# Optimization experiments

Measured on AMD Instinct MI355X. Metric: run time of the kernel, lower is better.

## Reference

```python
import jax, jax.numpy as jnp
import numpy as np

B = 16384
N_NODES = 55
N = B * N_NODES
IN_CH = 13
HID = 32
MAX_NBR = 6
N_LAYERS = 5
E = 4 * N


def _sage(x, src, dst, wl, bl, wr, n):
    # PyG SAGEConv: out = lin_l(mean_j x_j) + lin_r(x_i); lin_l has bias, lin_r does not.
    msgs = x[src]                                                   # [E, d]
    agg = jax.ops.segment_sum(msgs, dst, num_segments=n)            # [N, d]
    cnt = jax.ops.segment_sum(jnp.ones((src.shape[0],), x.dtype), dst, num_segments=n)
    agg = agg / jnp.maximum(cnt, 1.0)[:, None]
    return agg @ wl + bl + x @ wr


def setup_inputs() -> dict:
    key = jax.random.key(0)
    ks = jax.random.split(key, 24)
    x = jax.random.normal(ks[0], (N, IN_CH), dtype=jnp.float32)
    # column -3 (index 10) is a binary neighbor mask: exactly MAX_NBR ones per graph
    u = jax.random.uniform(ks[1], (B, N_NODES))
    nbr_idx = jnp.argsort(u, axis=1)[:, :MAX_NBR]
    mask = jnp.zeros((B, N_NODES), jnp.float32).at[jnp.arange(B)[:, None], nbr_idx].set(1.0)
    x = x.at[:, IN_CH - 3].set(mask.reshape(-1))
    edge_index = jax.random.randint(ks[2], (2, E), 0, N, dtype=jnp.int64)
    shuffle_indices = jax.random.randint(ks[3], (B, MAX_NBR), 0, MAX_NBR, dtype=jnp.int64)
    s = 0.1
    wl0 = jax.random.normal(ks[4], (IN_CH, HID)) * s
    bl0 = jnp.zeros((HID,), jnp.float32)
    wr0 = jax.random.normal(ks[5], (IN_CH, HID)) * s
    wl = jax.random.normal(ks[6], (N_LAYERS - 1, HID, HID)) * s
    bl = jnp.zeros((N_LAYERS - 1, HID), jnp.float32)
    wr = jax.random.normal(ks[7], (N_LAYERS - 1, HID, HID)) * s
    wq = jax.random.normal(ks[8], (HID, HID)) * s
    bq = jnp.zeros((HID,), jnp.float32)
    wk = jax.random.normal(ks[9], (HID, HID)) * s
    bk = jnp.zeros((HID,), jnp.float32)
    wv = jax.random.normal(ks[10], (HID, HID)) * s
    bv = jnp.zeros((HID,), jnp.float32)
    wo = jax.random.normal(ks[11], (HID, HID)) * s
    bo = jnp.zeros((HID,), jnp.float32)
    w_fc = jax.random.normal(ks[12], (HID * MAX_NBR, MAX_NBR)) * s
    b_fc = jnp.zeros((MAX_NBR,), jnp.float32)
    return {"x": x, "edge_index": edge_index, "shuffle_indices": shuffle_indices,
            "wl0": wl0, "bl0": bl0, "wr0": wr0, "wl": wl, "bl": bl, "wr": wr,
            "wq": wq, "bq": bq, "wk": wk, "bk": bk, "wv": wv, "bv": bv,
            "wo": wo, "bo": bo, "w_fc": w_fc, "b_fc": b_fc}


def reference(x, edge_index, shuffle_indices, wl0, bl0, wr0, wl, bl, wr,
              wq, bq, wk, bk, wv, bv, wo, bo, w_fc, b_fc):
    n = x.shape[0]
    b = n // N_NODES
    src, dst = edge_index[0], edge_index[1]
    nbr_mask = x[:, IN_CH - 3].reshape(b, N_NODES)                  # [B, 55]

    h = jax.nn.selu(_sage(x, src, dst, wl0, bl0, wr0, n))
    jk = h
    for i in range(N_LAYERS - 1):
        h = jax.nn.selu(_sage(h, src, dst, wl[i], bl[i], wr[i], n))
        jk = jnp.maximum(jk, h)                                     # JumpingKnowledge('max')

    h = jax.nn.selu(jk)                                             # [N, HID]
    keys = h.reshape(b, N_NODES, HID)
    values = keys

    # dynamic neighbor gather: indices of mask==1 in ascending order, zero-padded to MAX_NBR
    order = jnp.argsort(-nbr_mask, axis=1, stable=True)[:, :MAX_NBR]  # [B, 6]
    barange = jnp.arange(b)[:, None]
    query = keys[barange, order]                                    # [B, 6, HID]
    valid = jnp.take_along_axis(nbr_mask, order, axis=1) > 0.5      # [B, 6] bool
    query = jnp.where(valid[..., None], query, 0.0)
    query = query[barange, shuffle_indices]                         # shuffled gather

    # single-head cross attention (head_dim = HID)
    Q = query @ wq + bq
    K = keys @ wk + bk
    V = values @ wv + bv
    scores = jnp.einsum('bqd,bkd->bqk', Q, K) / jnp.sqrt(jnp.float32(HID))
    attn = jax.nn.softmax(scores, axis=-1)
    out = jnp.einsum('bqk,bkd->bqd', attn, V) @ wo + bo             # [B, 6, HID]

    out = jax.nn.selu(out.reshape(b, HID * MAX_NBR))
    return out @ w_fc + b_fc                                        # [B, 6]
```

## Files before the change

### kernel.cpp

```cpp
#include <hip/hip_runtime.h>
#include <cstdint>
#include <cstddef>

#define NODES   55
#define BGRAPH  16384
#define NTOT    (BGRAPH*NODES)
#define INCH    13
#define HID     32
#define ETOT    (4*NTOT)
#define NPB     128
#define ECAP    768
#define ZN      NTOT

#define NBUCK   220
#define BSH     12
#define BMSK    4095
#define NBLK    2048
#define BCAP2   32
#define BINTH   256
#define BINGRP  (ETOT/4/NBLK)
#define OVFCAP  8192

#define ASTR    72
#define BSTR    72
#define ASTR0   40

typedef _Float16 f16;
typedef _Float16 f16x4 __attribute__((ext_vector_type(4)));
typedef _Float16 f16x8 __attribute__((ext_vector_type(8)));
typedef float    f32x4 __attribute__((ext_vector_type(4)));

__device__ __forceinline__ float selu_f(float v){
  const float s  = 1.0507009873554805f;
  const float sa = 1.7580993408473766f;
  return v > 0.f ? s*v : sa*(__expf(v)-1.f);
}

__global__ __launch_bounds__(256) void k_pad(const float* __restrict__ x,
                                             float* __restrict__ xf,
                                             uint32_t* __restrict__ ha32,
                                             int* __restrict__ ocnt){
  if (blockIdx.x == 0){
    int t = threadIdx.x;
    if (t == 0) *ocnt = 0;
    if (t < 16)            xf[(size_t)ZN*16 + t] = 0.f;
    if (t >= 16 && t < 32) ha32[(size_t)ZN*16 + (t-16)] = 0u;
  }
  int i = blockIdx.x*256 + threadIdx.x;
  int node = i>>2, q = i&3;
  const float* r = x + (size_t)node*INCH + q*4;
  float4 v;
  v.x = r[0];
  v.y = (q<3) ? r[1] : 0.f;
  v.z = (q<3) ? r[2] : 0.f;
  v.w = (q<3) ? r[3] : 0.f;
  ((float4*)xf)[i] = v;
}

__global__ __launch_bounds__(256) void k_wprep(
    const float* __restrict__ wl0, const float* __restrict__ wr0,
    const float* __restrict__ wl,  const float* __restrict__ wr,
    f16* __restrict__ wcp)
{
  int t = threadIdx.x;
  for (int i=t; i<1024; i+=256){
    int oc = i>>5, k = i&31;
    float v = 0.f;
    if (k < 13)                 v = wl0[k*HID + oc];
    else if (k >= 16 && k < 29) v = wr0[(k-16)*HID + oc];
    wcp[oc*32 + k] = (f16)v;
  }
  for (int i=t; i<4*2048; i+=256){
    int l = i>>11, r = i&2047, oc = r>>6, k = r&63;
    float v = (k<32) ? wl[l*1024 + k*HID + oc] : wr[l*1024 + (k-32)*HID + oc];
    wcp[1024 + l*2048 + oc*64 + k] = (f16)v;
  }
}

__global__ __launch_bounds__(BINTH) void k_bin(
    const int* __restrict__ src, const int* __restrict__ dst,
    uint32_t* __restrict__ binned, int* __restrict__ gcnt,
    uint2* __restrict__ ovf, int* __restrict__ ocnt)
{
  __shared__ int lcnt[NBUCK];
  int t = threadIdx.x, bid = blockIdx.x;
  for (int i=t;i<NBUCK;i+=BINTH) lcnt[i]=0;
  __syncthreads();
  const int4* s4 = (const int4*)src;
  const int4* d4 = (const int4*)dst;
  int g0 = bid*BINGRP;
  for (int i=t; i<BINGRP; i+=BINTH){
    int4 s = s4[g0+i];
    int4 d = d4[g0+i];
    #pragma unroll
    for (int j=0;j<4;j++){
      int dd = (&d.x)[j];
      int ss = (&s.x)[j];
      int b  = dd >> BSH;
      uint32_t entry = (uint32_t)ss | ((uint32_t)(dd & BMSK) << 20);
      int pos = atomicAdd(&lcnt[b], 1);
      if (pos < BCAP2) binned[((size_t)b*NBLK + bid)*BCAP2 + pos] = entry;
      else {
        int gp = atomicAdd(ocnt, 1);
        if (gp < OVFCAP) ovf[gp] = make_uint2(entry, (uint32_t)b);
      }
    }
  }
  __syncthreads();
  for (int i=t;i<NBUCK;i+=BINTH){
    int c = lcnt[i]; if (c > BCAP2) c = BCAP2;
    gcnt[bid*NBUCK + i] = c;
  }
}

__global__ __launch_bounds__(256) void k_btot(const int* __restrict__ gcnt,
                                              const uint2* __restrict__ ovf,
                                              const int* __restrict__ ocnt,
                                              int* __restrict__ btot){
  __shared__ int sd[256];
  int b = blockIdx.x, t = threadIdx.x;
  int s = 0;
  for (int i=t;i<NBLK;i+=256) s += gcnt[i*NBUCK + b];
  int oc = *ocnt; if (oc > OVFCAP) oc = OVFCAP;
  for (int j=t;j<oc;j+=256) if (ovf[j].y == (uint32_t)b) s++;
  sd[t]=s; __syncthreads();
  for (int o=128;o>0;o>>=1){ if (t<o) sd[t]+=sd[t+o]; __syncthreads(); }
  if (t==0) btot[b]=sd[0];
}

__global__ __launch_bounds__(256) void k_bscan(const int* __restrict__ btot,
                                               int* __restrict__ bbase){
  __shared__ int sd[256];
  int t = threadIdx.x;
  int v = (t<NBUCK) ? btot[t] : 0;
  sd[t] = v; __syncthreads();
  for (int o=1;o<256;o<<=1){
    int u = (t>=o) ? sd[t-o] : 0;
    __syncthreads();
    sd[t] += u;
    __syncthreads();
  }
  if (t<NBUCK) bbase[t] = sd[t] - v;
}

__global__ __launch_bounds__(1024) void k_bucket(
    const uint32_t* __restrict__ binned, const int* __restrict__ gcnt,
    const int* __restrict__ bbase,
    const uint2* __restrict__ ovf, const int* __restrict__ ocnt,
    int* __restrict__ off, uint32_t* __restrict__ csrp)
{
  __shared__ int hist[4096];
  __shared__ int cnts[NBLK];
  __shared__ int ws[1024];
  int b = blockIdx.x, t = threadIdx.x;
  int base = bbase[b];
  for (int i=t;i<NBLK;i+=1024) cnts[i] = gcnt[i*NBUCK + b];
  #pragma unroll
  for (int i=0;i<4;i++) hist[t+1024*i] = 0;
  int oc = *ocnt; if (oc > OVFCAP) oc = OVFCAP;
  __syncthreads();

  const uint4* bb4 = (const uint4*)(binned + (size_t)b*(NBLK*BCAP2));
  for (int i=t; i<NBLK*BCAP2/4; i+=1024){
    uint4 e = bb4[i];
    int c = cnts[i>>3];
    int s0 = (i&7)*4;
    if (s0   < c) atomicAdd(&hist[(e.x>>20)&BMSK],1);
    if (s0+1 < c) atomicAdd(&hist[(e.y>>20)&BMSK],1);
    if (s0+2 < c) atomicAdd(&hist[(e.z>>20)&BMSK],1);
    if (s0+3 < c) atomicAdd(&hist[(e.w>>20)&BMSK],1);
  }
  for (int j=t;j<oc;j+=1024){
    uint2 pr = ovf[j];
    if (pr.y == (uint32_t)b) atomicAdd(&hist[(pr.x>>20)&BMSK],1);
  }
  __syncthreads();
  int t4 = t*4;
  int s0=hist[t4], s1=hist[t4+1], s2=hist[t4+2], s3=hist[t4+3];
  int sum = s0+s1+s2+s3;
  ws[t] = sum; __syncthreads();
  for (int o=1;o<1024;o<<=1){
    int u = (t>=o) ? ws[t-o] : 0;
    __syncthreads();
    ws[t] += u;
    __syncthreads();
  }
  int ex = ws[t] - sum;
  int p0 = ex, p1 = ex+s0, p2 = ex+s0+s1, p3 = ex+s0+s1+s2;
  hist[t4]=p0; hist[t4+1]=p1; hist[t4+2]=p2; hist[t4+3]=p3;
  int4 ov; ov.x = base+p0; ov.y = base+p1; ov.z = base+p2; ov.w = base+p3;
  ((int4*)(off + (b<<BSH)))[t] = ov;
  if (b == NBUCK-1 && t == 1023) off[NTOT] = ETOT;
  __syncthreads();
  for (int i=t; i<NBLK*BCAP2/4; i+=1024){
    uint4 e = bb4[i];
    int c = cnts[i>>3];
    int s0b = (i&7)*4;
    int p;
    if (s0b   < c){ p = atomicAdd(&hist[(e.x>>20)&BMSK],1); csrp[base+p] = e.x & 0xFFFFFu; }
    if (s0b+1 < c){ p = atomicAdd(&hist[(e.y>>20)&BMSK],1); csrp[base+p] = e.y & 0xFFFFFu; }
    if (s0b+2 < c){ p = atomicAdd(&hist[(e.z>>20)&BMSK],1); csrp[base+p] = e.z & 0xFFFFFu; }
    if (s0b+3 < c){ p = atomicAdd(&hist[(e.w>>20)&BMSK],1); csrp[base+p] = e.w & 0xFFFFFu; }
  }
  for (int j=t;j<oc;j+=1024){
    uint2 pr = ovf[j];
    if (pr.y == (uint32_t)b){
      int p = atomicAdd(&hist[(pr.x>>20)&BMSK],1);
      csrp[base+p] = pr.x & 0xFFFFFu;
    }
  }
}

__global__ __launch_bounds__(256,8) void k_layer0(
    const float* __restrict__ xf,
    const int* __restrict__ off, const uint32_t* __restrict__ csrp,
    const f16* __restrict__ wcat0, const float* __restrict__ bl0,
    f16* __restrict__ hout, f16* __restrict__ jkout)
{
  __shared__ uint32_t ALDS[NPB*(ASTR0/2)];
  __shared__ uint32_t BLDS[32*(ASTR0/2)];
  __shared__ uint32_t EL[ECAP];
  __shared__ int      sOFF[NPB+2];
  __shared__ float    biasL[32];
  int t = threadIdx.x;
  int base = blockIdx.x*NPB;
  int e0 = off[base];
  int e1 = off[base+NPB];
  for (int i=t; i<NPB+1; i+=256) sOFF[i] = off[base+i];
  {
    int lim = (e1-e0) < ECAP ? (e1-e0) : ECAP;
    for (int i=t; i<lim; i+=256) EL[i] = csrp[e0+i];
  }
  if (t < 128){
    int oc = t>>2, kq = (t&3)*8;
    f16x8 wv = *(const f16x8*)(wcat0 + oc*32 + kq);
    *(f16x8*)((f16*)BLDS + oc*ASTR0 + kq) = wv;
  }
  if (t < 32) biasL[t] = bl0[t];
  __syncthreads();

  int c4 = t & 3;
  #pragma unroll
  for (int p=0;p<2;p++){
    int nl = p*64 + (t>>2);
    int node = base + nl;
    float4 xown = *((const float4*)(xf + (size_t)node*16) + c4);
    int s = sOFF[nl] - e0;
    int d = sOFF[nl+1] - sOFF[nl];
    float a0=0.f,a1=0.f,a2=0.f,a3=0.f;
    for (int i=0;i<d;i+=4){
      int j0 = s+i;
      uint32_t k0,k1,k2,k3;
      if (j0+3 < ECAP){ k0=EL[j0]; k1=EL[j0+1]; k2=EL[j0+2]; k3=EL[j0+3]; }
      else            { k0=csrp[e0+j0]; k1=csrp[e0+j0+1]; k2=csrp[e0+j0+2]; k3=csrp[e0+j0+3]; }
      k1 = (i+1<d)?k1:(uint32_t)ZN;
      k2 = (i+2<d)?k2:(uint32_t)ZN;
      k3 = (i+3<d)?k3:(uint32_t)ZN;
      float4 g0 = *((const float4*)(xf + (size_t)k0*16u) + c4);
      float4 g1 = *((const float4*)(xf + (size_t)k1*16u) + c4);
      float4 g2 = *((const float4*)(xf + (size_t)k2*16u) + c4);
      float4 g3 = *((const float4*)(xf + (size_t)k3*16u) + c4);
      a0 += (g0.x+g1.x)+(g2.x+g3.x);
      a1 += (g0.y+g1.y)+(g2.y+g3.y);
      a2 += (g0.z+g1.z)+(g2.z+g3.z);
      a3 += (g0.w+g1.w)+(g2.w+g3.w);
    }
    float inv = 1.f/(float)(d<1?1:d);
    union { f16 h[4]; uint32_t u[2]; } mp, xp;
    mp.h[0]=(f16)(a0*inv); mp.h[1]=(f16)(a1*inv); mp.h[2]=(f16)(a2*inv); mp.h[3]=(f16)(a3*inv);
    xp.h[0]=(f16)xown.x;   xp.h[1]=(f16)xown.y;   xp.h[2]=(f16)xown.z;   xp.h[3]=(f16)xown.w;
    uint32_t* arow = &ALDS[nl*(ASTR0/2)];
    *((uint2*)&arow[2*c4])     = make_uint2(mp.u[0], mp.u[1]);
    *((uint2*)&arow[8 + 2*c4]) = make_uint2(xp.u[0], xp.u[1]);
  }
  __syncthreads();

  int w = t>>6, l = t&63;
  int lrow = l&15, lg = l>>4;
  const f16* Af = (const f16*)ALDS;
  const f16* Bf = (const f16*)BLDS;
  f32x4 D00={0.f,0.f,0.f,0.f}, D01=D00, D10=D00, D11=D00;
  {
    f16x8 af0 = *(const f16x8*)(Af + (32*w+lrow)*ASTR0    + 8*lg);
    f16x8 af1 = *(const f16x8*)(Af + (32*w+16+lrow)*ASTR0 + 8*lg);
    f16x8 bf0 = *(const f16x8*)(Bf + lrow*ASTR0           + 8*lg);
    f16x8 bf1 = *(const f16x8*)(Bf + (16+lrow)*ASTR0      + 8*lg);
    D00 = __builtin_amdgcn_mfma_f32_16x16x32_f16(af0, bf0, D00, 0,0,0);
    D01 = __builtin_amdgcn_mfma_f32_16x16x32_f16(af0, bf1, D01, 0,0,0);
    D10 = __builtin_amdgcn_mfma_f32_16x16x32_f16(af1, bf0, D10, 0,0,0);
    D11 = __builtin_amdgcn_mfma_f32_16x16x32_f16(af1, bf1, D11, 0,0,0);
  }
  __syncthreads();

  f16* ST = (f16*)ALDS;
  #pragma unroll
  for (int j=0;j<4;j++){
    int r0 = 32*w + 4*lg + j, r1 = r0 + 16;
    ST[r0*34 + lrow]      = (f16)selu_f(D00[j] + biasL[lrow]);
    ST[r0*34 + 16 + lrow] = (f16)selu_f(D01[j] + biasL[16+lrow]);
    ST[r1*34 + lrow]      = (f16)selu_f(D10[j] + biasL[lrow]);
    ST[r1*34 + 16 + lrow] = (f16)selu_f(D11[j] + biasL[16+lrow]);
  }
  __syncthreads();

  const uint32_t* STd = (const uint32_t*)ALDS;
  uint4* ho4 = (uint4*)hout;
  uint4* jo4 = (uint4*)jkout;
  int gbase = blockIdx.x*(NPB*HID/8);
  #pragma unroll
  for (int k=0;k<2;k++){
    int cch = t + 256*k;
    int n = cch>>2, m = cch&3;
    int dd = n*17 + m*4;
    uint4 u;
    u.x=STd[dd]; u.y=STd[dd+1]; u.z=STd[dd+2]; u.w=STd[dd+3];
    ho4[gbase+cch] = u;
    jo4[gbase+cch] = u;
  }
}

__global__ __launch_bounds__(256,6) void k_layer(
    const f16* __restrict__ hin,
    const int* __restrict__ off, const uint32_t* __restrict__ csrp,
    const f16* __restrict__ wcat, const float* __restrict__ bl,
    f16* __restrict__ hout, f16* __restrict__ jkio)
{
  __shared__ uint32_t ALDS[NPB*(ASTR/2)];
  __shared__ uint32_t BLDS[32*(BSTR/2)];
  __shared__ uint32_t EL[ECAP];
  __shared__ int      sOFF[NPB+2];
  __shared__ float    biasL[32];
  int t = threadIdx.x;
  int base = blockIdx.x*NPB;
  int e0 = off[base];
  int e1 = off[base+NPB];
  for (int i=t; i<NPB+1; i+=256) sOFF[i] = off[base+i];
  {
    int lim = (e1-e0) < ECAP ? (e1-e0) : ECAP;
    for (int i=t; i<lim; i+=256) EL[i] = csrp[e0+i];
  }
  if (t < 128){
    int oc = t>>2, kq = (t&3)*8;
    f16x8 wv0 = *(const f16x8*)(wcat + oc*64 + kq);
    f16x8 wv1 = *(const f16x8*)(wcat + oc*64 + 32 + kq);
    *(f16x8*)((f16*)BLDS + oc*BSTR + kq)      = wv0;
    *(f16x8*)((f16*)BLDS + oc*BSTR + 32 + kq) = wv1;
  }
  if (t < 32) biasL[t] = bl[t];
  __syncthreads();

  int c4 = t & 3;
  #pragma unroll
  for (int p=0;p<2;p++){
    int nl = p*64 + (t>>2);
    int node = base + nl;
    f16x8 hown = *(const f16x8*)(hin + (size_t)node*HID + 8u*c4);
    int s = sOFF[nl] - e0;
    int d = sOFF[nl+1] - sOFF[nl];
    float a[8];
    #pragma unroll
    for (int r=0;r<8;r++) a[r]=0.f;
    for (int i=0;i<d;i+=4){
      int j0 = s+i;
      uint32_t k0,k1,k2,k3;
      if (j0+3 < ECAP){ k0=EL[j0]; k1=EL[j0+1]; k2=EL[j0+2]; k3=EL[j0+3]; }
      else            { k0=csrp[e0+j0]; k1=csrp[e0+j0+1]; k2=csrp[e0+j0+2]; k3=csrp[e0+j0+3]; }
      k1 = (i+1<d)?k1:(uint32_t)ZN;
      k2 = (i+2<d)?k2:(uint32_t)ZN;
      k3 = (i+3<d)?k3:(uint32_t)ZN;
      f16x8 g0 = *((const f16x8*)(hin + (size_t)k0*32u) + c4);
      f16x8 g1 = *((const f16x8*)(hin + (size_t)k1*32u) + c4);
      f16x8 g2 = *((const f16x8*)(hin + (size_t)k2*32u) + c4);
      f16x8 g3 = *((const f16x8*)(hin + (size_t)k3*32u) + c4);
      #pragma unroll
      for (int r=0;r<8;r++)
        a[r] += ((float)g0[r]+(float)g1[r]) + ((float)g2[r]+(float)g3[r]);
    }
    float inv = 1.f/(float)(d<1?1:d);
    union { f16 h[8]; uint4 v; } mp;
    #pragma unroll
    for (int r=0;r<8;r++) mp.h[r] = (f16)(a[r]*inv);
    uint32_t* arow = &ALDS[nl*(ASTR/2)];
    *((uint4*)&arow[4*c4]) = mp.v;
    *((f16x8*)((f16*)arow + 32 + 8*c4)) = hown;
  }
  __syncthreads();

  int w = t>>6, l = t&63;
  int lrow = l&15, lg = l>>4;
  const f16* Af = (const f16*)ALDS;
  const f16* Bf = (const f16*)BLDS;
  f32x4 D00={0.f,0.f,0.f,0.f}, D01=D00, D10=D00, D11=D00;
  #pragma unroll
  for (int s2=0;s2<2;s2++){
    f16x8 af0 = *(const f16x8*)(Af + (32*w+lrow)*ASTR    + 32*s2 + 8*lg);
    f16x8 af1 = *(const f16x8*)(Af + (32*w+16+lrow)*ASTR + 32*s2 + 8*lg);
    f16x8 bf0 = *(const f16x8*)(Bf + lrow*BSTR           + 32*s2 + 8*lg);
    f16x8 bf1 = *(const f16x8*)(Bf + (16+lrow)*BSTR      + 32*s2 + 8*lg);
    D00 = __builtin_amdgcn_mfma_f32_16x16x32_f16(af0, bf0, D00, 0,0,0);
    D01 = __builtin_amdgcn_mfma_f32_16x16x32_f16(af0, bf1, D01, 0,0,0);
    D10 = __builtin_amdgcn_mfma_f32_16x16x32_f16(af1, bf0, D10, 0,0,0);
    D11 = __builtin_amdgcn_mfma_f32_16x16x32_f16(af1, bf1, D11, 0,0,0);
  }
  __syncthreads();

  f16* ST = (f16*)ALDS;
  #pragma unroll
  for (int j=0;j<4;j++){
    int r0 = 32*w + 4*lg + j, r1 = r0 + 16;
    ST[r0*34 + lrow]      = (f16)selu_f(D00[j] + biasL[lrow]);
    ST[r0*34 + 16 + lrow] = (f16)selu_f(D01[j] + biasL[16+lrow]);
    ST[r1*34 + lrow]      = (f16)selu_f(D10[j] + biasL[lrow]);
    ST[r1*34 + 16 + lrow] = (f16)selu_f(D11[j] + biasL[16+lrow]);
  }
  __syncthreads();

  const uint32_t* STd = (const uint32_t*)ALDS;
  uint4* ho4 = (uint4*)hout;
  uint4* jo4 = (uint4*)jkio;
  int gbase = blockIdx.x*(NPB*HID/8);
  #pragma unroll
  for (int k=0;k<2;k++){
    int cch = t + 256*k;
    int n = cch>>2, m = cch&3;
    int dd = n*17 + m*4;
    union { uint4 u; f16 hh[8]; } hv, jv;
    hv.u.x=STd[dd]; hv.u.y=STd[dd+1]; hv.u.z=STd[dd+2]; hv.u.w=STd[dd+3];
    jv.u = jo4[gbase+cch];
    #pragma unroll
    for (int r=0;r<8;r++){
      float a = (float)jv.hh[r], b = (float)hv.hh[r];
      jv.hh[r] = (f16)fmaxf(a, b);
    }
    ho4[gbase+cch] = hv.u;
    jo4[gbase+cch] = jv.u;
  }
}

__global__ __launch_bounds__(256) void k_attn(
    const f16* __restrict__ jk, const float* __restrict__ x,
    const int* __restrict__ shuf,
    const float* __restrict__ wq, const float* __restrict__ bq,
    const float* __restrict__ wk, const float* __restrict__ bk,
    const float* __restrict__ wv, const float* __restrict__ bv,
    const float* __restrict__ wo, const float* __restrict__ bo,
    const float* __restrict__ wfc, const float* __restrict__ bfc,
    float* __restrict__ out)
{
  __shared__ float H[NODES*33];
  __shared__ float K[NODES*33];
  __shared__ float V[NODES*33];
  __shared__ float Wq[HID*HID];
  __shared__ float Wo[HID*HID];
  __shared__ float Wfc[192*6];
  __shared__ float Qs[6*33];
  __shared__ float S[6*56];
  __shared__ float O[6*33];
  __shared__ float SO[192];
  __shared__ float part[96];
  __shared__ float M[NODES];
  __shared__ int order[8];
  __shared__ int sel[6];

  int g = blockIdx.x, t = threadIdx.x;
  for (int i=t; i<HID*HID; i+=256){ Wq[i]=wq[i]; Wo[i]=wo[i]; }
  for (int i=t; i<192*6;   i+=256){ Wfc[i]=wfc[i]; }
  {
    const f16x8* j8 = (const f16x8*)(jk + (size_t)g*NODES*HID);
    for (int i=t; i<NODES*HID/8; i+=256){
      f16x8 v = j8[i];
      int node = i >> 2, c0 = (i & 3)*8;
      #pragma unroll
      for (int r=0;r<8;r++) H[node*33 + c0 + r] = selu_f((float)v[r]);
    }
  }
  if (t < NODES) M[t] = x[(size_t)(g*NODES+t)*INCH + (INCH-3)];
  __syncthreads();
  if (t == 0){
    int c = 0;
    for (int n=0;n<NODES;n++) if (M[n] > 0.5f && c < 6) order[c++] = n;
  }
  __syncthreads();
  if (t < 6) sel[t] = order[shuf[g*6 + t]];
  __syncthreads();

  {
    int k = t & 63;
    int ocg = __builtin_amdgcn_readfirstlane(t >> 6);
    const float* wkp = wk + ocg*8;
    const float* wvp = wv + ocg*8;
    if (k < NODES){
      float ak[8], av[8];
      #pragma unroll
      for (int j=0;j<8;j++){ ak[j]=bk[ocg*8+j]; av[j]=bv[ocg*8+j]; }
      #pragma unroll
      for (int c=0;c<HID;c++){
        float hv = H[k*33+c];
        #pragma unroll
        for (int j=0;j<8;j++){
          ak[j] = fmaf(hv, wkp[c*HID+j], ak[j]);
          av[j] = fmaf(hv, wvp[c*HID+j], av[j]);
        }
      }
      #pragma unroll
      for (int j=0;j<8;j++){ K[k*33+ocg*8+j]=ak[j]; V[k*33+ocg*8+j]=av[j]; }
    }
  }
  if (t < 192){
    int q = t>>5, oc = t&31;
    int node = sel[q];
    float a = bq[oc];
    #pragma unroll
    for (int c=0;c<HID;c++) a = fmaf(H[node*33+c], Wq[c*HID+oc], a);
    Qs[q*33+oc] = a;
  }
  __syncthreads();

  for (int idx=t; idx<6*NODES; idx+=256){
    int q = idx % 6, k = idx / 6;
    float a = 0.f;
    #pragma unroll
    for (int c=0;c<HID;c++) a = fmaf(Qs[q*33+c], K[k*33+c], a);
    S[q*56+k] = a * 0.17677669529663687f;
  }
  __syncthreads();

  if (t < 192){
    int q = t>>5, l = t&31;
    float v0 = (l      < NODES) ? S[q*56+l]    : -1e30f;
    float v1 = (l+32   < NODES) ? S[q*56+l+32] : -1e30f;
    float mx = fmaxf(v0, v1);
    #pragma unroll
    for (int o=16;o>0;o>>=1) mx = fmaxf(mx, __shfl_xor(mx, o, 32));
    float p0 = (l    < NODES) ? __expf(v0-mx) : 0.f;
    float p1 = (l+32 < NODES) ? __expf(v1-mx) : 0.f;
    float sm = p0 + p1;
    #pragma unroll
    for (int o=16;o>0;o>>=1) sm += __shfl_xor(sm, o, 32);
    float inv = 1.f/sm;
    if (l    < NODES) S[q*56+l]    = p0*inv;
    if (l+32 < NODES) S[q*56+l+32] = p1*inv;
  }
  __syncthreads();

  if (t < 192){
    int q = t>>5, oc = t&31;
    float a = 0.f;
    for (int k=0;k<NODES;k++) a = fmaf(S[q*56+k], V[k*33+oc], a);
    O[q*33+oc] = a;
  }
  __syncthreads();

  if (t < 192){
    int q = t>>5, oc = t&31;
    float a = bo[oc];
    #pragma unroll
    for (int c=0;c<HID;c++) a = fmaf(O[q*33+c], Wo[c*HID+oc], a);
    SO[t] = selu_f(a);
  }
  __syncthreads();

  if (t < 96){
    int j = t % 6, pp = t / 6;
    float a = 0.f;
    #pragma unroll
    for (int r=0;r<12;r++) a = fmaf(SO[pp*12+r], Wfc[(pp*12+r)*6+j], a);
    part[pp*6+j] = a;
  }
  __syncthreads();
  if (t < 6){
    float a = bfc[t];
    #pragma unroll
    for (int pp=0;pp<16;pp++) a += part[pp*6+t];
    out[g*6+t] = a;
  }
}

extern "C" void kernel_launch(void* const* d_in, const int* in_sizes, int n_in,
                              void* d_out, int out_size, void* d_ws, size_t ws_size,
                              hipStream_t stream)
{
  const float* x   = (const float*)d_in[0];
  const int*   eix = (const int*)d_in[1];
  const int*   shf = (const int*)d_in[2];
  const float* wl0 = (const float*)d_in[3];
  const float* bl0 = (const float*)d_in[4];
  const float* wr0 = (const float*)d_in[5];
  const float* wl  = (const float*)d_in[6];
  const float* bl  = (const float*)d_in[7];
  const float* wr  = (const float*)d_in[8];
  const float* wq  = (const float*)d_in[9];
  const float* bq  = (const float*)d_in[10];
  const float* wk  = (const float*)d_in[11];
  const float* bk  = (const float*)d_in[12];
  const float* wv  = (const float*)d_in[13];
  const float* bv  = (const float*)d_in[14];
  const float* wo  = (const float*)d_in[15];
  const float* bo  = (const float*)d_in[16];
  const float* wfc = (const float*)d_in[17];
  const float* bfc = (const float*)d_in[18];
  float* out = (float*)d_out;

  const int* esrc = eix;
  const int* edst = eix + ETOT;

  char* p = (char*)d_ws;
  auto carve = [&](size_t bytes){ void* r = (void*)p; p += (bytes + 255) & ~(size_t)255; return r; };
  int*      off   = (int*)carve(sizeof(int)*(NTOT+1));
  int*      gcnt  = (int*)carve(sizeof(int)*(size_t)NBLK*NBUCK);
  int*      btot  = (int*)carve(sizeof(int)*256);
  int*      bbase = (int*)carve(sizeof(int)*256);
  uint2*    ovf   = (uint2*)carve(sizeof(uint2)*OVFCAP);
  int*      ocnt  = (int*)carve(sizeof(int)*64);
  f16*      wcp   = (f16*)carve(sizeof(f16)*(1024 + 4*2048));
  uint32_t* csrp  = (uint32_t*)carve(sizeof(uint32_t)*((size_t)ETOT + 64));
  f16*      h_a   = (f16*)carve(2*((size_t)NTOT+1)*HID);
  f16*      h_b   = (f16*)carve(2*((size_t)NTOT+1)*HID);
  f16*      jk16  = (f16*)carve(2*(size_t)NTOT*HID);

  float*    xf     = (float*)h_b;
  uint32_t* binned = (uint32_t*)h_a;

  k_pad   <<<ETOT/256,  256, 0, stream>>>(x, xf, (uint32_t*)h_a, ocnt);
  k_wprep <<<1,         256, 0, stream>>>(wl0, wr0, wl, wr, wcp);
  k_bin   <<<NBLK,    BINTH, 0, stream>>>(esrc, edst, binned, gcnt, ovf, ocnt);
  k_btot  <<<NBUCK,     256, 0, stream>>>(gcnt, ovf, ocnt, btot);
  k_bscan <<<1,         256, 0, stream>>>(btot, bbase);
  k_bucket<<<NBUCK,    1024, 0, stream>>>(binned, gcnt, bbase, ovf, ocnt, off, csrp);

  k_layer0<<<NTOT/NPB, 256, 0, stream>>>(xf, off, csrp, wcp, bl0, h_a, jk16);
  f16* hc = h_a; f16* hn = h_b;
  for (int l=0; l<4; l++){
    k_layer<<<NTOT/NPB, 256, 0, stream>>>(hc, off, csrp,
                                          wcp + 1024 + l*2048, bl + l*HID,
                                          hn, jk16);
    f16* tmp = hc; hc = hn; hn = tmp;
  }
  k_attn<<<BGRAPH, 256, 0, stream>>>(jk16, x, shf,
                                     wq, bq, wk, bk, wv, bv, wo, bo, wfc, bfc, out);
}
```

Baseline: 940.1 us.

## Use MFMA for attention K/V projection and ballot-based neighbor selection

Rewrites the per-graph attention kernel so the K and V projections run as f16 MFMA 16x16x32 tiles, using pre-transposed f16 Wk/Wv weights prepared in k_wprep. Hidden states are stored as f16 in shared memory, and neighbor selection now uses a wavefront ballot plus bit-clearing instead of a serial single-thread scan. Staging of Wq/Wo/Wfc into LDS is dropped in favour of direct global/cache reads. The aim is less LDS use, fewer barriers and less scalar FMA work per block, at the cost of f16 rounding in K/V and uncoalesced weight reads from cache.

```diff
diff --git a/kernel.cpp b/kernel.cpp
--- a/kernel.cpp
+++ b/kernel.cpp
@@ -24,6 +24,7 @@
 #define ASTR    72
 #define BSTR    72
 #define ASTR0   40
+#define WKV_OFF 9216
 
 typedef _Float16 f16;
 typedef _Float16 f16x4 __attribute__((ext_vector_type(4)));
@@ -60,6 +61,7 @@
 __global__ __launch_bounds__(256) void k_wprep(
     const float* __restrict__ wl0, const float* __restrict__ wr0,
     const float* __restrict__ wl,  const float* __restrict__ wr,
+    const float* __restrict__ wk,  const float* __restrict__ wv,
     f16* __restrict__ wcp)
 {
   int t = threadIdx.x;
@@ -74,6 +76,11 @@
     int l = i>>11, r = i&2047, oc = r>>6, k = r&63;
     float v = (k<32) ? wl[l*1024 + k*HID + oc] : wr[l*1024 + (k-32)*HID + oc];
     wcp[1024 + l*2048 + oc*64 + k] = (f16)v;
+  }
+  for (int i=t; i<2048; i+=256){
+    int oc = i>>5, k = i&31;
+    float v = (oc < 32) ? wk[k*HID + oc] : wv[k*HID + (oc-32)];
+    wcp[WKV_OFF + oc*32 + k] = (f16)v;
   }
 }
 
@@ -439,79 +446,77 @@
 
 __global__ __launch_bounds__(256) void k_attn(
     const f16* __restrict__ jk, const float* __restrict__ x,
-    const int* __restrict__ shuf,
+    const int* __restrict__ shuf, const f16* __restrict__ wkvT,
     const float* __restrict__ wq, const float* __restrict__ bq,
-    const float* __restrict__ wk, const float* __restrict__ bk,
-    const float* __restrict__ wv, const float* __restrict__ bv,
+    const float* __restrict__ bk, const float* __restrict__ bv,
     const float* __restrict__ wo, const float* __restrict__ bo,
     const float* __restrict__ wfc, const float* __restrict__ bfc,
     float* __restrict__ out)
 {
-  __shared__ float H[NODES*33];
+  __shared__ alignas(16) f16 Ah[64*40];
   __shared__ float K[NODES*33];
   __shared__ float V[NODES*33];
-  __shared__ float Wq[HID*HID];
-  __shared__ float Wo[HID*HID];
-  __shared__ float Wfc[192*6];
   __shared__ float Qs[6*33];
   __shared__ float S[6*56];
   __shared__ float O[6*33];
   __shared__ float SO[192];
   __shared__ float part[96];
-  __shared__ float M[NODES];
-  __shared__ int order[8];
-  __shared__ int sel[6];
+  __shared__ int   sel[8];
 
   int g = blockIdx.x, t = threadIdx.x;
-  for (int i=t; i<HID*HID; i+=256){ Wq[i]=wq[i]; Wo[i]=wo[i]; }
-  for (int i=t; i<192*6;   i+=256){ Wfc[i]=wfc[i]; }
+
   {
     const f16x8* j8 = (const f16x8*)(jk + (size_t)g*NODES*HID);
     for (int i=t; i<NODES*HID/8; i+=256){
       f16x8 v = j8[i];
       int node = i >> 2, c0 = (i & 3)*8;
+      f16x8 hv;
       #pragma unroll
-      for (int r=0;r<8;r++) H[node*33 + c0 + r] = selu_f((float)v[r]);
-    }
-  }
-  if (t < NODES) M[t] = x[(size_t)(g*NODES+t)*INCH + (INCH-3)];
-  __syncthreads();
-  if (t == 0){
-    int c = 0;
-    for (int n=0;n<NODES;n++) if (M[n] > 0.5f && c < 6) order[c++] = n;
-  }
-  __syncthreads();
-  if (t < 6) sel[t] = order[shuf[g*6 + t]];
+      for (int r=0;r<8;r++) hv[r] = (f16)selu_f((float)v[r]);
+      *(f16x8*)(Ah + node*40 + c0) = hv;
+    }
+  }
+  if (t < 64){
+    float mv = (t < NODES) ? x[(size_t)(g*NODES+t)*INCH + (INCH-3)] : 0.f;
+    unsigned long long mb = __ballot(mv > 0.5f);
+    if (t < 6){
+      int kk = shuf[g*6 + t];
+      for (int i2=0;i2<kk;i2++) mb &= (mb - 1ull);
+      sel[t] = (int)__builtin_ctzll(mb);
+    }
+  }
   __syncthreads();
 
   {
-    int k = t & 63;
-    int ocg = __builtin_amdgcn_readfirstlane(t >> 6);
-    const float* wkp = wk + ocg*8;
-    const float* wvp = wv + ocg*8;
-    if (k < NODES){
-      float ak[8], av[8];
+    int w = t>>6, l = t&63;
+    int lrow = l&15, lg = l>>4;
+    f16x8 af = *(const f16x8*)(Ah + (16*w + lrow)*40 + 8*lg);
+    #pragma unroll
+    for (int ct=0; ct<4; ct++){
+      f16x8 bf = *(const f16x8*)(wkvT + (16*ct + lrow)*32 + 8*lg);
+      f32x4 D = {0.f,0.f,0.f,0.f};
+      D = __builtin_amdgcn_mfma_f32_16x16x32_f16(af, bf, D, 0,0,0);
+      int ocl = 16*(ct&1) + lrow;
+      float bias = (ct < 2) ? bk[ocl] : bv[ocl];
+      float* dst = (ct < 2) ? K : V;
       #pragma unroll
-      for (int j=0;j<8;j++){ ak[j]=bk[ocg*8+j]; av[j]=bv[ocg*8+j]; }
-      #pragma unroll
-      for (int c=0;c<HID;c++){
-        float hv = H[k*33+c];
-        #pragma unroll
-        for (int j=0;j<8;j++){
-          ak[j] = fmaf(hv, wkp[c*HID+j], ak[j]);
-          av[j] = fmaf(hv, wvp[c*HID+j], av[j]);
-        }
+      for (int j=0;j<4;j++){
+        int node = 16*w + 4*lg + j;
+        if (node < NODES) dst[node*33 + ocl] = D[j] + bias;
       }
-      #pragma unroll
-      for (int j=0;j<8;j++){ K[k*33+ocg*8+j]=ak[j]; V[k*33+ocg*8+j]=av[j]; }
     }
   }
   if (t < 192){
     int q = t>>5, oc = t&31;
     int node = sel[q];
+    const f16x8* hr8 = (const f16x8*)(Ah + node*40);
     float a = bq[oc];
     #pragma unroll
-    for (int c=0;c<HID;c++) a = fmaf(H[node*33+c], Wq[c*HID+oc], a);
+    for (int cc=0;cc<4;cc++){
+      f16x8 hv = hr8[cc];
+      #pragma unroll
+      for (int r=0;r<8;r++) a = fmaf((float)hv[r], wq[(8*cc+r)*HID + oc], a);
+    }
     Qs[q*33+oc] = a;
   }
   __syncthreads();
@@ -555,7 +560,7 @@
     int q = t>>5, oc = t&31;
     float a = bo[oc];
     #pragma unroll
-    for (int c=0;c<HID;c++) a = fmaf(O[q*33+c], Wo[c*HID+oc], a);
+    for (int c=0;c<HID;c++) a = fmaf(O[q*33+c], wo[c*HID+oc], a);
     SO[t] = selu_f(a);
   }
   __syncthreads();
@@ -564,7 +569,7 @@
     int j = t % 6, pp = t / 6;
     float a = 0.f;
     #pragma unroll
-    for (int r=0;r<12;r++) a = fmaf(SO[pp*12+r], Wfc[(pp*12+r)*6+j], a);
+    for (int r=0;r<12;r++) a = fmaf(SO[pp*12+r], wfc[(pp*12+r)*6+j], a);
     part[pp*6+j] = a;
   }
   __syncthreads();
@@ -612,7 +617,7 @@
   int*      bbase = (int*)carve(sizeof(int)*256);
   uint2*    ovf   = (uint2*)carve(sizeof(uint2)*OVFCAP);
   int*      ocnt  = (int*)carve(sizeof(int)*64);
-  f16*      wcp   = (f16*)carve(sizeof(f16)*(1024 + 4*2048));
+  f16*      wcp   = (f16*)carve(sizeof(f16)*(WKV_OFF + 2048));
   uint32_t* csrp  = (uint32_t*)carve(sizeof(uint32_t)*((size_t)ETOT + 64));
   f16*      h_a   = (f16*)carve(2*((size_t)NTOT+1)*HID);
   f16*      h_b   = (f16*)carve(2*((size_t)NTOT+1)*HID);
@@ -622,7 +627,7 @@
   uint32_t* binned = (uint32_t*)h_a;
 
   k_pad   <<<ETOT/256,  256, 0, stream>>>(x, xf, (uint32_t*)h_a, ocnt);
-  k_wprep <<<1,         256, 0, stream>>>(wl0, wr0, wl, wr, wcp);
+  k_wprep <<<1,         256, 0, stream>>>(wl0, wr0, wl, wr, wk, wv, wcp);
   k_bin   <<<NBLK,    BINTH, 0, stream>>>(esrc, edst, binned, gcnt, ovf, ocnt);
   k_btot  <<<NBUCK,     256, 0, stream>>>(gcnt, ovf, ocnt, btot);
   k_bscan <<<1,         256, 0, stream>>>(btot, bbase);
@@ -636,6 +641,6 @@
                                           hn, jk16);
     f16* tmp = hc; hc = hn; hn = tmp;
   }
-  k_attn<<<BGRAPH, 256, 0, stream>>>(jk16, x, shf,
-                                     wq, bq, wk, bk, wv, bv, wo, bo, wfc, bfc, out);
-}
+  k_attn<<<BGRAPH, 256, 0, stream>>>(jk16, x, shf, wcp + WKV_OFF,
+                                     wq, bq, bk, bv, wo, bo, wfc, bfc, out);
+}
```

After: 841.2 us. -10.5%, faster.
